# Performance work log

Hardware: AMD Instinct MI355X
Metric: run time of the kernel (lower is better)

## Reference

```python
import jax, jax.numpy as jnp
import numpy as np

K = 3   # spatial_kernel_size
M = 5   # memory_size


def setup_inputs() -> dict:
    key = jax.random.key(0)
    ks = jax.random.split(key, 16)
    C = 64
    B, H, D, W = 2, 24, 24, 24
    s = 0.05
    n = jax.random.normal
    return {
        "x": n(ks[0], (B, C, H, D, W), jnp.float32),
        "prev_memory": jnp.zeros((B, C), jnp.float32),
        "Wq": n(ks[1], (C, C), jnp.float32) * s,
        "bq": n(ks[2], (C,), jnp.float32) * s,
        "Wk": n(ks[3], (C, C), jnp.float32) * s,
        "bk": n(ks[4], (C,), jnp.float32) * s,
        "Wv": n(ks[5], (C, C), jnp.float32) * s,
        "bv": n(ks[6], (C,), jnp.float32) * s,
        "mem_key": n(ks[7], (C, M), jnp.float32),
        "mem_value": n(ks[8], (C, M), jnp.float32),
        "Wg": n(ks[9], (C, 2 * C), jnp.float32) * s,
        "bg": n(ks[10], (C,), jnp.float32) * s,
        "W_ih": n(ks[11], (3 * C, C), jnp.float32) * s,
        "W_hh": n(ks[12], (3 * C, C), jnp.float32) * s,
        "b_ih": n(ks[13], (3 * C,), jnp.float32) * s,
        "b_hh": n(ks[14], (3 * C,), jnp.float32) * s,
    }


def _patches(x, k):
    # x: (B,C,H,D,W) -> (B,C,k^3,H,D,W) local neighborhoods (zero-padded)
    B, C, H, D, W = x.shape
    p = k // 2
    xp = jnp.pad(x, ((0, 0), (0, 0), (p, p), (p, p), (p, p)))
    sl = [xp[:, :, i:i + H, j:j + D, l:l + W]
          for i in range(k) for j in range(k) for l in range(k)]
    return jnp.stack(sl, axis=2)


def reference(x, prev_memory, Wq, bq, Wk, bk, Wv, bv, mem_key, mem_value,
              Wg, bg, W_ih, W_hh, b_ih, b_hh):
    B, C, H, D, W = x.shape
    N = H * D * W
    xf = x.reshape(B, C, N)
    pf = _patches(x, K).reshape(B, C, K ** 3, N)

    # 1x1x1 conv projections (pure channel mixes)
    q = jnp.einsum('oc,bcn->bon', Wq, xf) + bq[None, :, None]            # (B,C,N)
    k_sp = jnp.einsum('oc,bcmn->bomn', Wk, pf) + bk[None, :, None, None]  # (B,C,27,N)
    v_sp = jnp.einsum('oc,bcmn->bomn', Wv, pf) + bv[None, :, None, None]

    # memory tokens broadcast over all spatial locations
    k_mem = jnp.broadcast_to(mem_key[None, :, :, None], (B, C, M, N))
    v_mem = jnp.broadcast_to(mem_value[None, :, :, None], (B, C, M, N))
    kk = jnp.concatenate([k_mem, k_sp], axis=2)   # (B,C,M+27,N)
    vv = jnp.concatenate([v_mem, v_sp], axis=2)

    # per-channel scalar attention over memory+neighborhood axis
    attn = jax.nn.softmax(q[:, :, None, :] * kk / jnp.sqrt(jnp.float32(C)), axis=2)
    out = jnp.sum(attn * vv, axis=2).reshape(B, C, H, D, W)

    # sigmoid gate over concat([x, out])
    gin = jnp.concatenate([xf, out.reshape(B, C, N)], axis=1)  # (B,2C,N)
    gate = jax.nn.sigmoid(jnp.einsum('oc,bcn->bon', Wg, gin)
                          + bg[None, :, None]).reshape(B, C, H, D, W)
    out = gate * out + (1.0 - gate) * x

    # GRU memory update on spatially pooled features (torch GRUCell math)
    mu = out.mean(axis=(2, 3, 4))                 # (B,C)
    gi = mu @ W_ih.T + b_ih
    gh = prev_memory @ W_hh.T + b_hh
    ir, iz, ii = jnp.split(gi, 3, axis=1)
    hr, hz, hn = jnp.split(gh, 3, axis=1)
    r = jax.nn.sigmoid(ir + hr)
    z = jax.nn.sigmoid(iz + hz)
    ng = jnp.tanh(ii + r * hn)
    new_memory = (1.0 - z) * ng + z * prev_memory
    return out, new_memory
```

## Files before the change

### kernel.cpp

```cpp
#include <hip/hip_runtime.h>
#include <hip/hip_fp16.h>
#include <math.h>

#define NPOS 13824
#define CDIM 64
#define BTCH 2
#define LOG2E 1.4426950408889634f
#define QSCALE (0.125f * LOG2E)

typedef _Float16 f16;
typedef f16 f16x8 __attribute__((ext_vector_type(8)));
typedef float f32x4 __attribute__((ext_vector_type(4)));

__device__ __forceinline__ unsigned int f2bf1(float f) {
  unsigned int u = __float_as_uint(f);
  return (u + 0x7FFFu + ((u >> 16) & 1u)) >> 16;
}

__device__ __forceinline__ unsigned int pkh2(float a, float b) {
  __half2 h = __floats2half2_rn(a, b);
  return *reinterpret_cast<unsigned int*>(&h);
}

__global__ __launch_bounds__(256) void qkvg_kernel(
    const float* __restrict__ x,
    const float* __restrict__ Wq, const float* __restrict__ bq,
    const float* __restrict__ Wk, const float* __restrict__ bk,
    const float* __restrict__ Wv, const float* __restrict__ bv,
    const float* __restrict__ Wg,
    float* __restrict__ Qb, unsigned int* __restrict__ KVp,
    float* __restrict__ GXT, float* __restrict__ pool)
{
  __shared__ __align__(16) unsigned short ws[256*64];
  __shared__ __align__(16) unsigned short xs[64*64];
  const int t  = threadIdx.x;
  const int bi = blockIdx.x;
  const int b  = bi / 216;
  const int n0 = (bi - b*216) * 64;
  if (bi == 0 && t < 128) pool[t] = 0.0f;

  #pragma unroll
  for (int k = 0; k < 4; ++k) {
    const int u  = t + k*256;
    const int r  = u >> 4;
    const int i0 = (u & 15) * 4;
    const float4 q4 = *(const float4*)&Wq[r*64  + i0];
    const float4 g4 = *(const float4*)&Wg[r*128 + i0];
    const float4 k4 = *(const float4*)&Wk[r*64  + i0];
    const float4 v4 = *(const float4*)&Wv[r*64  + i0];
    {
      const int rr = r;
      const int idx = (rr*64 + i0) ^ ((rr & 7) << 3);
      *(uint2*)&ws[idx] = make_uint2(pkh2(q4.x*QSCALE, q4.y*QSCALE),
                                     pkh2(q4.z*QSCALE, q4.w*QSCALE));
    }
    {
      const int rr = 64 + r;
      const int idx = (rr*64 + i0) ^ ((rr & 7) << 3);
      *(uint2*)&ws[idx] = make_uint2(pkh2(g4.x, g4.y), pkh2(g4.z, g4.w));
    }
    {
      const int rr = 128 + 2*r;
      const int idx = (rr*64 + i0) ^ ((rr & 7) << 3);
      *(uint2*)&ws[idx] = make_uint2(pkh2(k4.x, k4.y), pkh2(k4.z, k4.w));
    }
    {
      const int rr = 129 + 2*r;
      const int idx = (rr*64 + i0) ^ ((rr & 7) << 3);
      *(uint2*)&ws[idx] = make_uint2(pkh2(v4.x, v4.y), pkh2(v4.z, v4.w));
    }
  }
  {
    const int p = t & 63;
    const size_t xb = (size_t)(b*64)*NPOS + n0 + p;
    #pragma unroll
    for (int k = 0; k < 8; ++k) {
      const int ch0 = (t >> 6) * 2 + k * 8;
      const float a0 = x[xb + (size_t)ch0*NPOS];
      const float a1 = x[xb + (size_t)(ch0+1)*NPOS];
      const int idx = (p*64 + ch0) ^ ((p & 7) << 3);
      *(unsigned int*)&xs[idx] = pkh2(a0, a1);
    }
  }
  __syncthreads();

  const int l   = t & 63;
  const int w   = t >> 6;
  const int lr  = l & 15;
  const int lkb = (l >> 4) * 8;
  const int swz = (lr & 7) << 3;

  f16x8 Bf[4][2];
  #pragma unroll
  for (int nf = 0; nf < 4; ++nf)
    #pragma unroll
    for (int kk = 0; kk < 2; ++kk) {
      const int prow = nf*16 + lr;
      Bf[nf][kk] = *(const f16x8*)&xs[(prow*64 + kk*32 + lkb) ^ swz];
    }
  f16x8 Af[4][2];
  #pragma unroll
  for (int f = 0; f < 4; ++f)
    #pragma unroll
    for (int kk = 0; kk < 2; ++kk) {
      const int row = (w*4 + f)*16 + lr;
      Af[f][kk] = *(const f16x8*)&ws[(row*64 + kk*32 + lkb) ^ swz];
    }
  f32x4 acc[4][4];
  #pragma unroll
  for (int f = 0; f < 4; ++f)
    #pragma unroll
    for (int nf = 0; nf < 4; ++nf) {
      f32x4 z = {0.f, 0.f, 0.f, 0.f};
      z = __builtin_amdgcn_mfma_f32_16x16x32_f16(Af[f][0], Bf[nf][0], z, 0, 0, 0);
      acc[f][nf] = __builtin_amdgcn_mfma_f32_16x16x32_f16(Af[f][1], Bf[nf][1], z, 0, 0, 0);
    }

  const int rsub  = (l >> 4) * 4;
  const int pbase = b*NPOS + n0;
  if (w == 0) {
    #pragma unroll
    for (int f = 0; f < 4; ++f) {
      const int ch0 = f*16 + rsub;
      const float4 bq4 = *(const float4*)&bq[ch0];
      #pragma unroll
      for (int nf = 0; nf < 4; ++nf) {
        const int p = pbase + nf*16 + lr;
        const float4 o = make_float4(fmaf(bq4.x, QSCALE, acc[f][nf].x),
                                     fmaf(bq4.y, QSCALE, acc[f][nf].y),
                                     fmaf(bq4.z, QSCALE, acc[f][nf].z),
                                     fmaf(bq4.w, QSCALE, acc[f][nf].w));
        *(float4*)&Qb[(size_t)p*64 + ch0] = o;
      }
    }
  } else if (w == 1) {
    #pragma unroll
    for (int f = 0; f < 4; ++f) {
      const int ch0 = f*16 + rsub;
      #pragma unroll
      for (int nf = 0; nf < 4; ++nf) {
        const int pl = n0 + nf*16 + lr;
        const int p  = pbase + nf*16 + lr;
        const float xv0 = x[(size_t)(b*64 + ch0+0)*NPOS + pl];
        const float xv1 = x[(size_t)(b*64 + ch0+1)*NPOS + pl];
        const float xv2 = x[(size_t)(b*64 + ch0+2)*NPOS + pl];
        const float xv3 = x[(size_t)(b*64 + ch0+3)*NPOS + pl];
        const float4 o0 = make_float4(acc[f][nf].x, xv0, acc[f][nf].y, xv1);
        const float4 o1 = make_float4(acc[f][nf].z, xv2, acc[f][nf].w, xv3);
        *(float4*)&GXT[((size_t)p*64 + ch0)*2]     = o0;
        *(float4*)&GXT[((size_t)p*64 + ch0)*2 + 4] = o1;
      }
    }
  } else {
    #pragma unroll
    for (int f = 0; f < 4; ++f) {
      const int c0 = (w - 2)*32 + f*8 + (l >> 4)*2;
      const float2 bk2 = *(const float2*)&bk[c0];
      const float2 bv2 = *(const float2*)&bv[c0];
      #pragma unroll
      for (int nf = 0; nf < 4; ++nf) {
        const int p = pbase + nf*16 + lr;
        uint2 kv;
        kv.x = (f2bf1(acc[f][nf].x + bk2.x) << 16) | f2bf1(acc[f][nf].y + bv2.x);
        kv.y = (f2bf1(acc[f][nf].z + bk2.y) << 16) | f2bf1(acc[f][nf].w + bv2.y);
        *(uint2*)&KVp[(size_t)p*64 + c0] = kv;
      }
    }
  }
}

__global__ __launch_bounds__(256, 4) void attn_kernel(
    float* __restrict__ QOT,
    const unsigned int* __restrict__ KVp,
    const float* __restrict__ GXT,
    const float* __restrict__ bk, const float* __restrict__ bv,
    const float* __restrict__ memk, const float* __restrict__ memv,
    const float* __restrict__ Wg, const float* __restrict__ bg,
    float* __restrict__ pool)
{
  __shared__ __align__(16) unsigned int kvbuf2[64*127 + 128];
  __shared__ __align__(16) float alsA[256];
  __shared__ __align__(16) float alsB[256];
  const int t = threadIdx.x;
  const int c = t & 63;
  const int w = t >> 6;

  {
    float* wgt2 = (float*)kvbuf2;
    #pragma unroll
    for (int k = 0; k < 16; ++k) {
      int u = t + k*256;
      int cp = u >> 6, j = u & 63;
      wgt2[j*65 + cp] = Wg[cp*128 + 64 + j];
    }
  }
  __syncthreads();
  unsigned int wg2p[32];
  {
    const float* wgt2 = (const float*)kvbuf2;
    #pragma unroll
    for (int j2 = 0; j2 < 32; ++j2) {
      unsigned lo = f2bf1(wgt2[(2*j2)*65 + c]);
      unsigned hi = f2bf1(wgt2[(2*j2+1)*65 + c]);
      wg2p[j2] = lo | (hi << 16);
    }
  }
  float mk[5], mv[5];
  #pragma unroll
  for (int m = 0; m < 5; ++m) { mk[m] = memk[c*5 + m]; mv[m] = memv[c*5 + m]; }
  const float bg_c = bg[c];
  __syncthreads();

  const int bi = (int)(blockIdx.x & 7) * 128 + (int)(blockIdx.x >> 3);
  const int b  = bi >> 9;
  const int tb = bi & 511;
  const int h0 = (tb >> 6) * 3;
  const int d0 = ((tb >> 3) & 7) * 3;
  const int w0 = (tb & 7) * 3;
  const int bN = b * NPOS;

  for (int u = t; u < 125*16; u += 256) {
    int pos = u >> 4, q4 = u & 15;
    int ph = pos / 25, pr = pos - ph*25;
    int pd = pr / 5,  pw = pr - pd*5;
    int hh = h0 - 1 + ph, dd = d0 - 1 + pd, ww = w0 - 1 + pw;
    bool inb = ((unsigned)hh < 24u) && ((unsigned)dd < 24u) && ((unsigned)ww < 24u);
    uint4 kv;
    if (inb) {
      kv = *(const uint4*)(KVp + ((size_t)(bN + hh*576 + dd*24 + ww))*64 + q4*4);
    } else {
      const float4 kf = ((const float4*)bk)[q4];
      const float4 vf = ((const float4*)bv)[q4];
      kv.x = (f2bf1(kf.x) << 16) | f2bf1(vf.x);
      kv.y = (f2bf1(kf.y) << 16) | f2bf1(vf.y);
      kv.z = (f2bf1(kf.z) << 16) | f2bf1(vf.z);
      kv.w = (f2bf1(kf.w) << 16) | f2bf1(vf.w);
    }
    kvbuf2[(4*q4 + 0)*127 + pos] = kv.x;
    kvbuf2[(4*q4 + 1)*127 + pos] = kv.y;
    kvbuf2[(4*q4 + 2)*127 + pos] = kv.z;
    kvbuf2[(4*q4 + 3)*127 + pos] = kv.w;
  }
  __syncthreads();

  float pacc = 0.0f;
  for (int li = w; li < 27; li += 8) {
    const int liB0 = li + 4;
    const bool hasB = liB0 < 27;
    const int liB = hasB ? liB0 : li;

    const int lhA = li / 9,  lrA = li - lhA*9;
    const int ldA = lrA / 3, lwA = lrA - ldA*3;
    const int pA  = bN + (h0+lhA)*576 + (d0+ldA)*24 + (w0+lwA);
    const int hbA = c*127 + lhA*25 + ldA*5 + lwA;
    const int lhB = liB / 9,  lrB = liB - lhB*9;
    const int ldB = lrB / 3,  lwB = lrB - ldB*3;
    const int pB  = bN + (h0+lhB)*576 + (d0+ldB)*24 + (w0+lwB);
    const int hbB = c*127 + lhB*25 + ldB*5 + lwB;

    const float qA = QOT[pA*64 + c];
    const float qB = QOT[pB*64 + c];
    const float2 gxA = *(const float2*)&GXT[(size_t)(pA*64 + c)*2];
    const float2 gxB = *(const float2*)&GXT[(size_t)(pB*64 + c)*2];

    float sA0 = 0.f, sA1 = 0.f, oA0 = 0.f, oA1 = 0.f;
    float sB0 = 0.f, sB1 = 0.f, oB0 = 0.f, oB1 = 0.f;
    #pragma unroll
    for (int m = 0; m < 5; ++m) {
      const float pfA = __builtin_amdgcn_exp2f(qA * mk[m]);
      const float pfB = __builtin_amdgcn_exp2f(qB * mk[m]);
      if (m & 1) { sA1 += pfA; oA1 = fmaf(pfA, mv[m], oA1);
                   sB1 += pfB; oB1 = fmaf(pfB, mv[m], oB1); }
      else       { sA0 += pfA; oA0 = fmaf(pfA, mv[m], oA0);
                   sB0 += pfB; oB0 = fmaf(pfB, mv[m], oB0); }
    }
    const unsigned int* kvA = &kvbuf2[hbA];
    const unsigned int* kvB = &kvbuf2[hbB];
    #pragma unroll
    for (int i = 0; i < 3; ++i)
      #pragma unroll
      for (int j = 0; j < 3; ++j)
        #pragma unroll
        for (int l = 0; l < 3; ++l) {
          const int s4  = i*9 + j*3 + l;
          const int off = i*25 + j*5 + l;
          const unsigned a = kvA[off], bb2 = kvB[off];
          const float kA = __uint_as_float(a & 0xFFFF0000u);
          const float vA = __uint_as_float(a << 16);
          const float kB = __uint_as_float(bb2 & 0xFFFF0000u);
          const float vB = __uint_as_float(bb2 << 16);
          const float pfA = __builtin_amdgcn_exp2f(qA * kA);
          const float pfB = __builtin_amdgcn_exp2f(qB * kB);
          if (s4 & 1) { sA1 += pfA; oA1 = fmaf(pfA, vA, oA1);
                        sB1 += pfB; oB1 = fmaf(pfB, vB, oB1); }
          else        { sA0 += pfA; oA0 = fmaf(pfA, vA, oA0);
                        sB0 += pfB; oB0 = fmaf(pfB, vB, oB0); }
        }
    const float attA = (oA0 + oA1) * __builtin_amdgcn_rcpf(sA0 + sA1);
    const float attB = (oB0 + oB1) * __builtin_amdgcn_rcpf(sB0 + sB1);

    alsA[w*64 + c] = attA;
    alsB[w*64 + c] = attB;
    float gA0 = gxA.x + bg_c, gA1 = 0.f, gA2 = 0.f, gA3 = 0.f;
    float gB0 = gxB.x + bg_c, gB1 = 0.f, gB2 = 0.f, gB3 = 0.f;
    #pragma unroll
    for (int j4 = 0; j4 < 16; ++j4) {
      const float4 a4 = *(const float4*)&alsA[w*64 + j4*4];
      const float4 b4 = *(const float4*)&alsB[w*64 + j4*4];
      const unsigned pk0 = wg2p[2*j4], pk1 = wg2p[2*j4+1];
      const float w0f = __uint_as_float(pk0 << 16);
      const float w1f = __uint_as_float(pk0 & 0xFFFF0000u);
      const float w2f = __uint_as_float(pk1 << 16);
      const float w3f = __uint_as_float(pk1 & 0xFFFF0000u);
      gA0 = fmaf(w0f, a4.x, gA0); gB0 = fmaf(w0f, b4.x, gB0);
      gA1 = fmaf(w1f, a4.y, gA1); gB1 = fmaf(w1f, b4.y, gB1);
      gA2 = fmaf(w2f, a4.z, gA2); gB2 = fmaf(w2f, b4.z, gB2);
      gA3 = fmaf(w3f, a4.w, gA3); gB3 = fmaf(w3f, b4.w, gB3);
    }
    const float glA   = (gA0 + gA1) + (gA2 + gA3);
    const float glB   = (gB0 + gB1) + (gB2 + gB3);
    const float gateA = __builtin_amdgcn_rcpf(1.0f + __builtin_amdgcn_exp2f(-LOG2E * glA));
    const float gateB = __builtin_amdgcn_rcpf(1.0f + __builtin_amdgcn_exp2f(-LOG2E * glB));
    const float finA  = fmaf(gateA, attA - gxA.y, gxA.y);
    const float finB  = fmaf(gateB, attB - gxB.y, gxB.y);
    QOT[pA*64 + c] = finA;
    pacc += finA;
    if (hasB) { QOT[pB*64 + c] = finB; pacc += finB; }
  }

  alsA[t] = pacc;
  __syncthreads();
  if (t < 64) {
    float s = alsA[t] + alsA[64 + t] + alsA[128 + t] + alsA[192 + t];
    atomicAdd(&pool[b*64 + t], s);
  }
}

__global__ __launch_bounds__(256) void outpool_kernel(
    const float* __restrict__ OT, float* __restrict__ out,
    const float* __restrict__ pool, const float* __restrict__ prev,
    const float* __restrict__ W_ih, const float* __restrict__ W_hh,
    const float* __restrict__ b_ih, const float* __restrict__ b_hh,
    float* __restrict__ outmem)
{
  __shared__ __align__(16) float ls[64*65];
  __shared__ __align__(16) float mu[128];
  __shared__ float gi[384];
  __shared__ float gh[384];
  const int t  = threadIdx.x;
  const int bi = blockIdx.x;
  const int b  = bi / 216;
  const int n0 = (bi - b*216) * 64;
  #pragma unroll
  for (int i = 0; i < 16; ++i) {
    int u = i*256 + t;
    int pos = u >> 6, cc = u & 63;
    ls[cc*65 + pos] = OT[(size_t)(b*NPOS + n0 + pos)*64 + cc];
  }
  if (bi == 0 && t < 128) mu[t] = pool[t] * (1.0f / (float)NPOS);
  __syncthreads();
  #pragma unroll
  for (int i = 0; i < 16; ++i) {
    int u = i*256 + t;
    int cc = u >> 6, j = u & 63;
    out[(size_t)(b*64 + cc)*NPOS + n0 + j] = ls[cc*65 + j];
  }
  if (bi != 0) return;

  for (int r = t; r < 384; r += 256) {
    const int b2 = r / 192, j = r - b2*192;
    const float4* wi4 = (const float4*)(W_ih + (size_t)j*64);
    const float4* wh4 = (const float4*)(W_hh + (size_t)j*64);
    const float4* mu4 = (const float4*)(mu + b2*64);
    const float4* pv4 = (const float4*)(prev + b2*64);
    float sgi = b_ih[j], sgh = b_hh[j];
    #pragma unroll
    for (int k = 0; k < 16; ++k) {
      float4 wv = wi4[k], m4 = mu4[k];
      sgi = fmaf(wv.x, m4.x, sgi); sgi = fmaf(wv.y, m4.y, sgi);
      sgi = fmaf(wv.z, m4.z, sgi); sgi = fmaf(wv.w, m4.w, sgi);
      float4 hv = wh4[k], p4 = pv4[k];
      sgh = fmaf(hv.x, p4.x, sgh); sgh = fmaf(hv.y, p4.y, sgh);
      sgh = fmaf(hv.z, p4.z, sgh); sgh = fmaf(hv.w, p4.w, sgh);
    }
    gi[r] = sgi; gh[r] = sgh;
  }
  __syncthreads();
  if (t < 128) {
    const int b2 = t >> 6, cc = t & 63;
    float ir = gi[b2*192 + cc],       hr = gh[b2*192 + cc];
    float iz = gi[b2*192 + 64 + cc],  hz = gh[b2*192 + 64 + cc];
    float ii = gi[b2*192 + 128 + cc], hn = gh[b2*192 + 128 + cc];
    float rr = 1.0f / (1.0f + __builtin_amdgcn_exp2f(-LOG2E * (ir + hr)));
    float zz = 1.0f / (1.0f + __builtin_amdgcn_exp2f(-LOG2E * (iz + hz)));
    float ng = tanhf(ii + rr * hn);
    outmem[t] = (1.0f - zz) * ng + zz * prev[t];
  }
}

extern "C" void kernel_launch(void* const* d_in, const int* in_sizes, int n_in,
                              void* d_out, int out_size, void* d_ws, size_t ws_size,
                              hipStream_t stream) {
  const float* x    = (const float*)d_in[0];
  const float* prev = (const float*)d_in[1];
  const float* Wq   = (const float*)d_in[2];
  const float* bq   = (const float*)d_in[3];
  const float* Wk   = (const float*)d_in[4];
  const float* bk   = (const float*)d_in[5];
  const float* Wv   = (const float*)d_in[6];
  const float* bv   = (const float*)d_in[7];
  const float* memk = (const float*)d_in[8];
  const float* memv = (const float*)d_in[9];
  const float* Wg   = (const float*)d_in[10];
  const float* bg   = (const float*)d_in[11];
  const float* W_ih = (const float*)d_in[12];
  const float* W_hh = (const float*)d_in[13];
  const float* b_ih = (const float*)d_in[14];
  const float* b_hh = (const float*)d_in[15];

  float* out    = (float*)d_out;
  float* outmem = out + (size_t)BTCH*CDIM*NPOS;

  const size_t SZ = (size_t)BTCH*NPOS*CDIM;
  float* wsf       = (float*)d_ws;
  float* Qb        = wsf;
  unsigned int* KVp = (unsigned int*)(wsf + SZ);
  float* GXT       = wsf + 2*SZ;
  float* pool      = wsf + 4*SZ;

  qkvg_kernel<<<BTCH*216, 256, 0, stream>>>(x, Wq, bq, Wk, bk, Wv, bv, Wg,
                                            Qb, KVp, GXT, pool);
  attn_kernel<<<BTCH*512, 256, 0, stream>>>(Qb, KVp, GXT,
                                            bk, bv, memk, memv, Wg, bg, pool);
  outpool_kernel<<<BTCH*216, 256, 0, stream>>>(Qb, out, pool, prev,
                                               W_ih, W_hh, b_ih, b_hh, outmem);
}
```

Baseline: 139.7 us.

## Move gate matmul into output kernel with MFMA and store intermediates in fp16

```diff
diff --git a/kernel.cpp b/kernel.cpp
--- a/kernel.cpp
+++ b/kernel.cpp
@@ -10,6 +10,7 @@
 
 typedef _Float16 f16;
 typedef f16 f16x8 __attribute__((ext_vector_type(8)));
+typedef f16 f16x4 __attribute__((ext_vector_type(4)));
 typedef float f32x4 __attribute__((ext_vector_type(4)));
 
 __device__ __forceinline__ unsigned int f2bf1(float f) {
@@ -27,9 +28,9 @@
     const float* __restrict__ Wq, const float* __restrict__ bq,
     const float* __restrict__ Wk, const float* __restrict__ bk,
     const float* __restrict__ Wv, const float* __restrict__ bv,
-    const float* __restrict__ Wg,
-    float* __restrict__ Qb, unsigned int* __restrict__ KVp,
-    float* __restrict__ GXT, float* __restrict__ pool)
+    const float* __restrict__ Wg, const float* __restrict__ bg,
+    f16* __restrict__ Qh, unsigned int* __restrict__ KVp,
+    f16* __restrict__ G1h, float* __restrict__ pool)
 {
   __shared__ __align__(16) unsigned short ws[256*64];
   __shared__ __align__(16) unsigned short xs[64*64];
@@ -37,7 +38,7 @@
   const int bi = blockIdx.x;
   const int b  = bi / 216;
   const int n0 = (bi - b*216) * 64;
-  if (bi == 0 && t < 128) pool[t] = 0.0f;
+  if (bi == 0 && t < 132) pool[t] = 0.0f;
 
   #pragma unroll
   for (int k = 0; k < 4; ++k) {
@@ -126,29 +127,26 @@
       #pragma unroll
       for (int nf = 0; nf < 4; ++nf) {
         const int p = pbase + nf*16 + lr;
-        const float4 o = make_float4(fmaf(bq4.x, QSCALE, acc[f][nf].x),
-                                     fmaf(bq4.y, QSCALE, acc[f][nf].y),
-                                     fmaf(bq4.z, QSCALE, acc[f][nf].z),
-                                     fmaf(bq4.w, QSCALE, acc[f][nf].w));
-        *(float4*)&Qb[(size_t)p*64 + ch0] = o;
+        uint2 o;
+        o.x = pkh2(fmaf(bq4.x, QSCALE, acc[f][nf].x),
+                   fmaf(bq4.y, QSCALE, acc[f][nf].y));
+        o.y = pkh2(fmaf(bq4.z, QSCALE, acc[f][nf].z),
+                   fmaf(bq4.w, QSCALE, acc[f][nf].w));
+        *(uint2*)&Qh[(size_t)p*64 + ch0] = o;
       }
     }
   } else if (w == 1) {
     #pragma unroll
     for (int f = 0; f < 4; ++f) {
       const int ch0 = f*16 + rsub;
+      const float4 bg4 = *(const float4*)&bg[ch0];
       #pragma unroll
       for (int nf = 0; nf < 4; ++nf) {
-        const int pl = n0 + nf*16 + lr;
-        const int p  = pbase + nf*16 + lr;
-        const float xv0 = x[(size_t)(b*64 + ch0+0)*NPOS + pl];
-        const float xv1 = x[(size_t)(b*64 + ch0+1)*NPOS + pl];
-        const float xv2 = x[(size_t)(b*64 + ch0+2)*NPOS + pl];
-        const float xv3 = x[(size_t)(b*64 + ch0+3)*NPOS + pl];
-        const float4 o0 = make_float4(acc[f][nf].x, xv0, acc[f][nf].y, xv1);
-        const float4 o1 = make_float4(acc[f][nf].z, xv2, acc[f][nf].w, xv3);
-        *(float4*)&GXT[((size_t)p*64 + ch0)*2]     = o0;
-        *(float4*)&GXT[((size_t)p*64 + ch0)*2 + 4] = o1;
+        const int p = pbase + nf*16 + lr;
+        uint2 o;
+        o.x = pkh2(acc[f][nf].x + bg4.x, acc[f][nf].y + bg4.y);
+        o.y = pkh2(acc[f][nf].z + bg4.z, acc[f][nf].w + bg4.w);
+        *(uint2*)&G1h[(size_t)p*64 + ch0] = o;
       }
     }
   } else {
@@ -170,46 +168,20 @@
 }
 
 __global__ __launch_bounds__(256, 4) void attn_kernel(
-    float* __restrict__ QOT,
+    const f16* __restrict__ Qh,
     const unsigned int* __restrict__ KVp,
-    const float* __restrict__ GXT,
+    f16* __restrict__ ATTh,
     const float* __restrict__ bk, const float* __restrict__ bv,
-    const float* __restrict__ memk, const float* __restrict__ memv,
-    const float* __restrict__ Wg, const float* __restrict__ bg,
-    float* __restrict__ pool)
+    const float* __restrict__ memk, const float* __restrict__ memv)
 {
-  __shared__ __align__(16) unsigned int kvbuf2[64*127 + 128];
-  __shared__ __align__(16) float alsA[256];
-  __shared__ __align__(16) float alsB[256];
+  __shared__ __align__(16) unsigned int kvbuf2[64*127 + 64];
   const int t = threadIdx.x;
   const int c = t & 63;
   const int w = t >> 6;
 
-  {
-    float* wgt2 = (float*)kvbuf2;
-    #pragma unroll
-    for (int k = 0; k < 16; ++k) {
-      int u = t + k*256;
-      int cp = u >> 6, j = u & 63;
-      wgt2[j*65 + cp] = Wg[cp*128 + 64 + j];
-    }
-  }
-  __syncthreads();
-  unsigned int wg2p[32];
-  {
-    const float* wgt2 = (const float*)kvbuf2;
-    #pragma unroll
-    for (int j2 = 0; j2 < 32; ++j2) {
-      unsigned lo = f2bf1(wgt2[(2*j2)*65 + c]);
-      unsigned hi = f2bf1(wgt2[(2*j2+1)*65 + c]);
-      wg2p[j2] = lo | (hi << 16);
-    }
-  }
   float mk[5], mv[5];
   #pragma unroll
   for (int m = 0; m < 5; ++m) { mk[m] = memk[c*5 + m]; mv[m] = memv[c*5 + m]; }
-  const float bg_c = bg[c];
-  __syncthreads();
 
   const int bi = (int)(blockIdx.x & 7) * 128 + (int)(blockIdx.x >> 3);
   const int b  = bi >> 9;
@@ -243,7 +215,6 @@
   }
   __syncthreads();
 
-  float pacc = 0.0f;
   for (int li = w; li < 27; li += 8) {
     const int liB0 = li + 4;
     const bool hasB = liB0 < 27;
@@ -258,10 +229,8 @@
     const int pB  = bN + (h0+lhB)*576 + (d0+ldB)*24 + (w0+lwB);
     const int hbB = c*127 + lhB*25 + ldB*5 + lwB;
 
-    const float qA = QOT[pA*64 + c];
-    const float qB = QOT[pB*64 + c];
-    const float2 gxA = *(const float2*)&GXT[(size_t)(pA*64 + c)*2];
-    const float2 gxB = *(const float2*)&GXT[(size_t)(pB*64 + c)*2];
+    const float qA = (float)Qh[(size_t)pA*64 + c];
+    const float qB = (float)Qh[(size_t)pB*64 + c];
 
     float sA0 = 0.f, sA1 = 0.f, oA0 = 0.f, oA1 = 0.f;
     float sB0 = 0.f, sB1 = 0.f, oB0 = 0.f, oB1 = 0.f;
@@ -281,9 +250,9 @@
       #pragma unroll
       for (int j = 0; j < 3; ++j)
         #pragma unroll
-        for (int l = 0; l < 3; ++l) {
-          const int s4  = i*9 + j*3 + l;
-          const int off = i*25 + j*5 + l;
+        for (int l2 = 0; l2 < 3; ++l2) {
+          const int s4  = i*9 + j*3 + l2;
+          const int off = i*25 + j*5 + l2;
           const unsigned a = kvA[off], bb2 = kvB[off];
           const float kA = __uint_as_float(a & 0xFFFF0000u);
           const float vA = __uint_as_float(a << 16);
@@ -298,75 +267,129 @@
         }
     const float attA = (oA0 + oA1) * __builtin_amdgcn_rcpf(sA0 + sA1);
     const float attB = (oB0 + oB1) * __builtin_amdgcn_rcpf(sB0 + sB1);
-
-    alsA[w*64 + c] = attA;
-    alsB[w*64 + c] = attB;
-    float gA0 = gxA.x + bg_c, gA1 = 0.f, gA2 = 0.f, gA3 = 0.f;
-    float gB0 = gxB.x + bg_c, gB1 = 0.f, gB2 = 0.f, gB3 = 0.f;
-    #pragma unroll
-    for (int j4 = 0; j4 < 16; ++j4) {
-      const float4 a4 = *(const float4*)&alsA[w*64 + j4*4];
-      const float4 b4 = *(const float4*)&alsB[w*64 + j4*4];
-      const unsigned pk0 = wg2p[2*j4], pk1 = wg2p[2*j4+1];
-      const float w0f = __uint_as_float(pk0 << 16);
-      const float w1f = __uint_as_float(pk0 & 0xFFFF0000u);
-      const float w2f = __uint_as_float(pk1 << 16);
-      const float w3f = __uint_as_float(pk1 & 0xFFFF0000u);
-      gA0 = fmaf(w0f, a4.x, gA0); gB0 = fmaf(w0f, b4.x, gB0);
-      gA1 = fmaf(w1f, a4.y, gA1); gB1 = fmaf(w1f, b4.y, gB1);
-      gA2 = fmaf(w2f, a4.z, gA2); gB2 = fmaf(w2f, b4.z, gB2);
-      gA3 = fmaf(w3f, a4.w, gA3); gB3 = fmaf(w3f, b4.w, gB3);
-    }
-    const float glA   = (gA0 + gA1) + (gA2 + gA3);
-    const float glB   = (gB0 + gB1) + (gB2 + gB3);
-    const float gateA = __builtin_amdgcn_rcpf(1.0f + __builtin_amdgcn_exp2f(-LOG2E * glA));
-    const float gateB = __builtin_amdgcn_rcpf(1.0f + __builtin_amdgcn_exp2f(-LOG2E * glB));
-    const float finA  = fmaf(gateA, attA - gxA.y, gxA.y);
-    const float finB  = fmaf(gateB, attB - gxB.y, gxB.y);
-    QOT[pA*64 + c] = finA;
-    pacc += finA;
-    if (hasB) { QOT[pB*64 + c] = finB; pacc += finB; }
-  }
-
-  alsA[t] = pacc;
-  __syncthreads();
-  if (t < 64) {
-    float s = alsA[t] + alsA[64 + t] + alsA[128 + t] + alsA[192 + t];
-    atomicAdd(&pool[b*64 + t], s);
-  }
-}
-
-__global__ __launch_bounds__(256) void outpool_kernel(
-    const float* __restrict__ OT, float* __restrict__ out,
-    const float* __restrict__ pool, const float* __restrict__ prev,
+    ATTh[(size_t)pA*64 + c] = (f16)attA;
+    if (hasB) ATTh[(size_t)pB*64 + c] = (f16)attB;
+  }
+}
+
+__global__ __launch_bounds__(256) void outgate_kernel(
+    const f16* __restrict__ ATTh, const f16* __restrict__ G1h,
+    const float* __restrict__ x, const float* __restrict__ Wg,
+    float* __restrict__ out,
+    float* __restrict__ pool, const float* __restrict__ prev,
     const float* __restrict__ W_ih, const float* __restrict__ W_hh,
     const float* __restrict__ b_ih, const float* __restrict__ b_hh,
     float* __restrict__ outmem)
 {
-  __shared__ __align__(16) float ls[64*65];
-  __shared__ __align__(16) float mu[128];
+  __shared__ __align__(16) unsigned short wgs[64*64];
+  __shared__ __align__(16) f16 att_s[64*64];
+  __shared__ __align__(16) f16 g1_s[64*64];
+  __shared__ __align__(16) float xf_s[64*65];
+  __shared__ __align__(16) float red[256];
+  __shared__ float mu[128];
   __shared__ float gi[384];
   __shared__ float gh[384];
+  __shared__ unsigned int lastf;
   const int t  = threadIdx.x;
   const int bi = blockIdx.x;
   const int b  = bi / 216;
   const int n0 = (bi - b*216) * 64;
+  unsigned int* counter = (unsigned int*)(pool + 128);
+
+  #pragma unroll
+  for (int k = 0; k < 4; ++k) {
+    const int u  = t + k*256;
+    const int r  = u >> 4;
+    const int i0 = (u & 15) * 4;
+    const float4 g4 = *(const float4*)&Wg[r*128 + 64 + i0];
+    const int idx = (r*64 + i0) ^ ((r & 7) << 3);
+    *(uint2*)&wgs[idx] = make_uint2(pkh2(g4.x, g4.y), pkh2(g4.z, g4.w));
+  }
+  {
+    const unsigned int* attu = (const unsigned int*)(ATTh + (size_t)(b*NPOS + n0)*64);
+    const unsigned int* g1u  = (const unsigned int*)(G1h  + (size_t)(b*NPOS + n0)*64);
+    #pragma unroll
+    for (int k = 0; k < 8; ++k) {
+      const int u = t + k*256;
+      const int p = u >> 5, c2 = u & 31;
+      ((unsigned int*)att_s)[(p*32 + c2) ^ ((p & 7) << 2)] = attu[u];
+      ((unsigned int*)g1_s)[u] = g1u[u];
+    }
+  }
+  #pragma unroll
+  for (int k = 0; k < 16; ++k) {
+    const int u = t + k*256;
+    const int cc = u >> 6, pp = u & 63;
+    xf_s[pp*65 + cc] = x[(size_t)(b*64 + cc)*NPOS + n0 + pp];
+  }
+  __syncthreads();
+
+  const int l   = t & 63;
+  const int w   = t >> 6;
+  const int lr  = l & 15;
+  const int lkb = (l >> 4) * 8;
+  const int swz = (lr & 7) << 3;
+  f16x8 Aw[2];
+  #pragma unroll
+  for (int kk = 0; kk < 2; ++kk) {
+    const int row = w*16 + lr;
+    Aw[kk] = *(const f16x8*)&wgs[(row*64 + kk*32 + lkb) ^ swz];
+  }
+  f32x4 acc[4];
+  #pragma unroll
+  for (int nf = 0; nf < 4; ++nf) {
+    f16x8 B0 = *(const f16x8*)&att_s[(((nf*16 + lr)*64) + 0*32 + lkb) ^ swz];
+    f16x8 B1 = *(const f16x8*)&att_s[(((nf*16 + lr)*64) + 1*32 + lkb) ^ swz];
+    f32x4 z = {0.f, 0.f, 0.f, 0.f};
+    z = __builtin_amdgcn_mfma_f32_16x16x32_f16(Aw[0], B0, z, 0, 0, 0);
+    acc[nf] = __builtin_amdgcn_mfma_f32_16x16x32_f16(Aw[1], B1, z, 0, 0, 0);
+  }
+
+  const int c0 = w*16 + (l >> 4)*4;
+  #pragma unroll
+  for (int nf = 0; nf < 4; ++nf) {
+    const int pl  = nf*16 + lr;
+    const f16x4 av = *(const f16x4*)&att_s[(pl*64 + c0) ^ ((pl & 7) << 3)];
+    const f16x4 gv = *(const f16x4*)&g1_s[pl*64 + c0];
+    #pragma unroll
+    for (int e = 0; e < 4; ++e) {
+      const float attv  = (float)av[e];
+      const float logit = acc[nf][e] + (float)gv[e];
+      const float gate  = __builtin_amdgcn_rcpf(1.0f + __builtin_amdgcn_exp2f(-LOG2E * logit));
+      const float xv    = xf_s[pl*65 + c0 + e];
+      xf_s[pl*65 + c0 + e] = fmaf(gate, attv - xv, xv);
+    }
+  }
+  __syncthreads();
+
   #pragma unroll
   for (int i = 0; i < 16; ++i) {
-    int u = i*256 + t;
-    int pos = u >> 6, cc = u & 63;
-    ls[cc*65 + pos] = OT[(size_t)(b*NPOS + n0 + pos)*64 + cc];
-  }
-  if (bi == 0 && t < 128) mu[t] = pool[t] * (1.0f / (float)NPOS);
-  __syncthreads();
-  #pragma unroll
-  for (int i = 0; i < 16; ++i) {
-    int u = i*256 + t;
-    int cc = u >> 6, j = u & 63;
-    out[(size_t)(b*64 + cc)*NPOS + n0 + j] = ls[cc*65 + j];
-  }
-  if (bi != 0) return;
-
+    const int u = i*256 + t;
+    const int cc = u >> 6, j = u & 63;
+    out[(size_t)(b*64 + cc)*NPOS + n0 + j] = xf_s[j*65 + cc];
+  }
+  {
+    const int q = t >> 6, cc = t & 63;
+    float s = 0.f;
+    #pragma unroll
+    for (int p2 = 0; p2 < 16; ++p2) s += xf_s[(q*16 + p2)*65 + cc];
+    red[t] = s;
+  }
+  __syncthreads();
+  if (t < 64) {
+    const float s = red[t] + red[64 + t] + red[128 + t] + red[192 + t];
+    atomicAdd(&pool[b*64 + t], s);
+  }
+  __syncthreads();
+  if (t == 0) {
+    __threadfence();
+    lastf = (atomicAdd(counter, 1u) == (unsigned)(BTCH*216 - 1)) ? 1u : 0u;
+  }
+  __syncthreads();
+  if (!lastf) return;
+
+  if (t < 128) mu[t] = atomicAdd(&pool[t], 0.0f) * (1.0f / (float)NPOS);
+  __syncthreads();
   for (int r = t; r < 384; r += 256) {
     const int b2 = r / 192, j = r - b2*192;
     const float4* wi4 = (const float4*)(W_ih + (size_t)j*64);
@@ -422,16 +445,17 @@
   float* outmem = out + (size_t)BTCH*CDIM*NPOS;
 
   const size_t SZ = (size_t)BTCH*NPOS*CDIM;
-  float* wsf       = (float*)d_ws;
-  float* Qb        = wsf;
-  unsigned int* KVp = (unsigned int*)(wsf + SZ);
-  float* GXT       = wsf + 2*SZ;
-  float* pool      = wsf + 4*SZ;
-
-  qkvg_kernel<<<BTCH*216, 256, 0, stream>>>(x, Wq, bq, Wk, bk, Wv, bv, Wg,
-                                            Qb, KVp, GXT, pool);
-  attn_kernel<<<BTCH*512, 256, 0, stream>>>(Qb, KVp, GXT,
-                                            bk, bv, memk, memv, Wg, bg, pool);
-  outpool_kernel<<<BTCH*216, 256, 0, stream>>>(Qb, out, pool, prev,
+  float* wsf        = (float*)d_ws;
+  f16*  Qh          = (f16*)wsf;
+  unsigned int* KVp = (unsigned int*)(wsf + SZ/2);
+  f16*  G1h         = (f16*)(wsf + SZ/2 + SZ);
+  f16*  ATTh        = (f16*)(wsf + 2*SZ);
+  float* pool       = wsf + 2*SZ + SZ/2;
+
+  qkvg_kernel<<<BTCH*216, 256, 0, stream>>>(x, Wq, bq, Wk, bk, Wv, bv, Wg, bg,
+                                            Qh, KVp, G1h, pool);
+  attn_kernel<<<BTCH*512, 256, 0, stream>>>(Qh, KVp, ATTh,
+                                            bk, bv, memk, memv);
+  outgate_kernel<<<BTCH*216, 256, 0, stream>>>(ATTh, G1h, x, Wg, out, pool, prev,
                                                W_ih, W_hh, b_ih, b_hh, outmem);
 }
```

After: 141.5 us. About the same (+1.2%).
